# Performance work log

Measured on AMD Instinct MI355X. Metric: run time of the kernel, lower is better.

The kernel has to match this reference:

```python
import jax, jax.numpy as jnp
import numpy as np


def setup_inputs() -> dict:
    key = jax.random.key(0)
    kx, kh = jax.random.split(key)
    x = jax.random.normal(kx, (32, 4, 131072), dtype=jnp.float32)
    h = jax.random.normal(kh, (32, 4, 32768), dtype=jnp.float32)
    return {"x": x, "h": h}


def reference(x, h):
    # Causal FFT convolution: convolve(x, h, mode='causal', pad_mode='min').
    x_len = x.shape[-1]
    h_len = h.shape[-1]
    pad_len = x_len + h_len - 1  # pad_mode='min'
    # rfft with n=pad_len == zero-pad to pad_len then rfft (matches F.pad + rfft)
    X = jnp.fft.rfft(x, n=pad_len)
    H = jnp.fft.rfft(h, n=pad_len)
    Y = X * H
    # torch.fft.irfft default output length = 2*(n_freq-1); jnp matches this default.
    y_pad = jnp.fft.irfft(Y)
    # 'causal' mode: keep first x_len samples
    return y_pad[..., :x_len]
```

## Files before the change

### kernel.cpp

```cpp
#include <hip/hip_runtime.h>
#include <hip/hip_fp16.h>


#define L1FFT 262144
#define NCHAN 128
#define CN1 163839LL
#define CN2 163838LL
#define MBINS 81920
#define XLEN 131072
#define HLEN 32768
#define TWO_PI 6.28318530717958647692f
#define INV512T (1.0f/512.0f)
#define INVLT   (1.0f/262144.0f)
#define CHIRP12 ((float)(0.5 / (163839.0 * 163838.0)))

#define CM_BUILD   0
#define CM_REAL    1
#define CM_COMBINE 2
#define CM_EXTRACT 3
#define CM_FINAL   4
#define RM_BUILD   0
#define RM_CONV    1

#define TS  518
#define TFS 261

typedef float cplx __attribute__((ext_vector_type(2)));

__device__ __forceinline__ cplx mkc(float x, float y){ cplx r; r.x = x; r.y = y; return r; }
__device__ __forceinline__ cplx cmulf(cplx a, cplx b) {
  return a.xx*b + a.yy*mkc(-b.y, b.x);
}
__device__ __forceinline__ cplx cmulcf(cplx a, cplx b) {
  return a.yy*b.yx + a.xx*mkc(b.x, -b.y);
}
__device__ __forceinline__ cplx crot(cplx t, float dsg) {
  return mkc(-dsg*t.y, dsg*t.x);
}

__device__ __forceinline__ cplx sc_turn(float t) {
  return mkc(__builtin_amdgcn_cosf(t), __builtin_amdgcn_sinf(t));
}

__device__ __forceinline__ cplx chirp1(float sgn, long long n) {
  long long m = (n*n) % (2*CN1);
  return sc_turn(sgn * (float)m * (1.0f/(float)(2*CN1)));
}
__device__ __forceinline__ cplx chirp2(float sgn, long long n) {
  long long m = (n*n) % (2*CN2);
  return sc_turn(sgn * (float)m * (1.0f/(float)(2*CN2)));
}
__device__ __forceinline__ cplx chirpv(float sgn, long long Q, long long n) {
  long long m = (n*n) % (2*Q);
  float ang = sgn * (0.5f*TWO_PI) * (float)m / (float)Q;
  float s, c; __sincosf(ang, &s, &c);
  return mkc(c, s);
}

__device__ __forceinline__ int brev4(int x) {
  return ((x&1)<<3) | ((x&2)<<1) | ((x&4)>>1) | ((x&8)>>3);
}
__device__ __forceinline__ int brev5(int x) {
  return (int)(__brev((unsigned)x) >> 27);
}

template<int M>
__device__ __forceinline__ float shf1f(float x) {
  if constexpr (M == 1) {
    return __int_as_float(__builtin_amdgcn_mov_dpp(__float_as_int(x), 0xB1, 0xF, 0xF, true));
  } else if constexpr (M == 2) {
    return __int_as_float(__builtin_amdgcn_mov_dpp(__float_as_int(x), 0x4E, 0xF, 0xF, true));
  } else if constexpr (M == 8) {
    return __int_as_float(__builtin_amdgcn_mov_dpp(__float_as_int(x), 0x128, 0xF, 0xF, true));
  } else {
    return __int_as_float(__builtin_amdgcn_ds_swizzle(__float_as_int(x), (M << 10) | 0x1F));
  }
}
template<int M>
__device__ __forceinline__ cplx shflxT(cplx a) {
  return mkc(shf1f<M>(a.x), shf1f<M>(a.y));
}

__device__ __forceinline__ cplx h2c(__half2 h) {
  float2 f = __half22float2(h); return mkc(f.x, f.y);
}
__device__ __forceinline__ __half2 c2h(cplx c) {
  return __float22half2_rn(make_float2(c.x, c.y));
}

#define C16_1 0.9238795325f
#define C16_2 0.7071067812f
#define C16_3 0.3826834324f
__device__ __forceinline__ float c16t(int j) {
  const float C[8] = {1.f, C16_1, C16_2, C16_3, 0.f, -C16_3, -C16_2, -C16_1};
  return C[j];
}
__device__ __forceinline__ float s16t(int j) {
  const float S[8] = {0.f, C16_3, C16_2, C16_1, 1.f, C16_1, C16_2, C16_3};
  return S[j];
}

__device__ __forceinline__ void lane16_fwd_rest(cplx v[16], float dsg) {
  #pragma unroll
  for (int h = 0; h < 2; ++h)
    #pragma unroll
    for (int j = 0; j < 4; ++j) {
      int i0 = h*8 + j;
      cplx w = mkc(c16t(2*j), dsg * s16t(2*j));
      cplx a = v[i0], b = v[i0+4];
      v[i0] = a + b;
      v[i0+4] = cmulf(a - b, w);
    }
  #pragma unroll
  for (int q = 0; q < 4; ++q)
    #pragma unroll
    for (int j = 0; j < 2; ++j) {
      int i0 = q*4 + j;
      cplx a = v[i0], b = v[i0+2];
      cplx tt = a - b;
      v[i0] = a + b;
      v[i0+2] = (j == 0) ? tt : crot(tt, dsg);
    }
  #pragma unroll
  for (int p = 0; p < 8; ++p) {
    cplx a = v[2*p], b = v[2*p+1];
    v[2*p] = a + b;
    v[2*p+1] = a - b;
  }
}
__device__ __forceinline__ void lane16_fwd(cplx v[16], float dsg) {
  #pragma unroll
  for (int j = 0; j < 8; ++j) {
    cplx w = mkc(c16t(j), dsg * s16t(j));
    cplx a = v[j], b = v[j+8];
    v[j] = a + b;
    v[j+8] = cmulf(a - b, w);
  }
  lane16_fwd_rest(v, dsg);
}
__device__ __forceinline__ void lane16_fwd_h0(cplx v[16], float dsg) {
  #pragma unroll
  for (int j = 0; j < 8; ++j) {
    cplx w = mkc(c16t(j), dsg * s16t(j));
    v[j+8] = cmulf(v[j], w);
  }
  lane16_fwd_rest(v, dsg);
}

__device__ __forceinline__ void lane16_inv(cplx v[16], float dsg) {
  #pragma unroll
  for (int p = 0; p < 8; ++p) {
    cplx a = v[2*p], b = v[2*p+1];
    v[2*p] = a + b;
    v[2*p+1] = a - b;
  }
  #pragma unroll
  for (int q = 0; q < 4; ++q)
    #pragma unroll
    for (int j = 0; j < 2; ++j) {
      int i0 = q*4 + j;
      cplx a = v[i0], b = v[i0+2];
      cplx tb = (j == 0) ? b : crot(b, -dsg);
      v[i0] = a + tb;
      v[i0+2] = a - tb;
    }
  #pragma unroll
  for (int h = 0; h < 2; ++h)
    #pragma unroll
    for (int j = 0; j < 4; ++j) {
      int i0 = h*8 + j;
      cplx w = mkc(c16t(2*j), dsg * s16t(2*j));
      cplx a = v[i0], b = v[i0+4];
      cplx tb = cmulcf(b, w);
      v[i0] = a + tb;
      v[i0+4] = a - tb;
    }
  #pragma unroll
  for (int j = 0; j < 8; ++j) {
    cplx w = mkc(c16t(j), dsg * s16t(j));
    cplx a = v[j], b = v[j+8];
    cplx tb = cmulcf(b, w);
    v[j] = a + tb;
    v[j+8] = a - tb;
  }
}

struct WSel { cplx a16, a8, a4, a2; };
__device__ __forceinline__ WSel make_wsel(int l, float dsg) {
  const cplx one = mkc(1.f, 0.f);
  WSel w;
  w.a16 = (l & 16) ? sc_turn(dsg * (1.0f/32.0f) * (float)(l & 15)) : one;
  w.a8  = (l & 8)  ? sc_turn(dsg * (1.0f/16.0f) * (float)(l & 7))  : one;
  w.a4  = (l & 4)  ? sc_turn(dsg * (1.0f/8.0f)  * (float)(l & 3))  : one;
  w.a2  = ((l & 2) && (l & 1)) ? mkc(0.f, dsg) : one;
  return w;
}

#define XF(mask, w) {                                                          \
    const float s_ = ((l & (mask)) != 0) ? -1.f : 1.f;                         \
    _Pragma("unroll")                                                          \
    for (int r = 0; r < 16; ++r) {                                             \
      cplx o = shflxT<(mask)>(v[r]);                                           \
      v[r] = cmulf(o + s_*v[r], (w));                                          \
    } }
#define XFP(mask) {                                                            \
    const float s_ = ((l & (mask)) != 0) ? -1.f : 1.f;                         \
    _Pragma("unroll")                                                          \
    for (int r = 0; r < 16; ++r) {                                             \
      cplx o = shflxT<(mask)>(v[r]);                                           \
      v[r] = o + s_*v[r];                                                      \
    } }
#define XI(mask, w) {                                                          \
    const float s_ = ((l & (mask)) != 0) ? -1.f : 1.f;                         \
    _Pragma("unroll")                                                          \
    for (int r = 0; r < 16; ++r) {                                             \
      cplx b = cmulcf(v[r], (w));                                              \
      cplx o = shflxT<(mask)>(b);                                              \
      v[r] = o + s_*b;                                                         \
    } }
#define XIP(mask) {                                                            \
    const float s_ = ((l & (mask)) != 0) ? -1.f : 1.f;                         \
    _Pragma("unroll")                                                          \
    for (int r = 0; r < 16; ++r) {                                             \
      cplx b = v[r];                                                           \
      cplx o = shflxT<(mask)>(b);                                              \
      v[r] = o + s_*b;                                                         \
    } }

#define TW_APPLY_FWD(rr, wexpr) v[rr] = cmulf(v[rr], (wexpr));
#define TW_APPLY_INV(rr, wexpr) v[rr] = cmulcf(v[rr], (wexpr));
#define TW512_BODY(APPLY)                                                      \
  cplx w1 = sc_turn(dsg * INV512T * (float)l);                                 \
  cplx w2 = cmulf(w1, w1);                                                     \
  cplx w3 = cmulf(w2, w1);                                                     \
  cplx w4 = cmulf(w2, w2);                                                     \
  cplx w8 = cmulf(w4, w4);                                                     \
  cplx w12 = cmulf(w8, w4);                                                    \
  APPLY(8, w1)  APPLY(4, w2)  APPLY(12, w3) APPLY(2, w4)                       \
  APPLY(10, cmulf(w4, w1)) APPLY(6, cmulf(w4, w2)) APPLY(14, cmulf(w4, w3))    \
  APPLY(1, w8)  APPLY(9, cmulf(w8, w1)) APPLY(5, cmulf(w8, w2))                \
  APPLY(13, cmulf(w8, w3)) APPLY(3, w12) APPLY(11, cmulf(w12, w1))             \
  APPLY(7, cmulf(w12, w2)) APPLY(15, cmulf(w12, w3))

__device__ __forceinline__ void twiddle512_fwd(cplx v[16], int l, float dsg) {
  TW512_BODY(TW_APPLY_FWD)
}
__device__ __forceinline__ void twiddle512_inv(cplx v[16], int l, float dsg) {
  TW512_BODY(TW_APPLY_INV)
}

__device__ __forceinline__ void fft512_core_fwd(cplx v[16], int l, float dsg,
                                                const WSel& w) {
  twiddle512_fwd(v, l, dsg);
  XF(16, w.a16); XF(8, w.a8); XF(4, w.a4); XF(2, w.a2); XFP(1);
}
__device__ __forceinline__ void fft512_fwd(cplx v[16], int l, float dsg,
                                           const WSel& w) {
  lane16_fwd(v, dsg);
  fft512_core_fwd(v, l, dsg, w);
}
__device__ __forceinline__ void fft512_fwd_h0(cplx v[16], int l, float dsg,
                                              const WSel& w) {
  lane16_fwd_h0(v, dsg);
  fft512_core_fwd(v, l, dsg, w);
}

__device__ __forceinline__ void fft512_inv(cplx v[16], int l, float dsg,
                                           const WSel& w) {
  XIP(1); XI(2, w.a2); XI(4, w.a4); XI(8, w.a8); XI(16, w.a16);
  twiddle512_inv(v, l, dsg);
  lane16_inv(v, dsg);
}


__global__ __launch_bounds__(256) void pass_col_k(
    int mode,
    const float* __restrict__ realSrc, int realLen,
    const __half2* cplxSrc,
    const __half2* __restrict__ hcIn,
    __half2* dstFull,
    __half2* __restrict__ specOut,
    float* __restrict__ realOut,
    long long Q, float csgn, int lo, int hi)
{
  __shared__ __align__(16) unsigned char ldsraw[8 * TS * 4];
  __half2* tile = (__half2*)ldsraw;
  const int t   = threadIdx.x;
  const int c0  = blockIdx.x * 8;
  const int ch  = blockIdx.y;
  const int l   = t & 31;
  const int ccf = t >> 5;
  const int c   = c0 + ccf;
  cplx v[16];
  WSel ws = make_wsel(l, -1.f);

  if (mode == CM_BUILD) {
    #pragma unroll
    for (int m = 0; m < 16; ++m) {
      int n = ((l + 32*m) << 9) + c;
      int np = (n <= hi) ? n : n - L1FFT;
      v[m] = (np >= lo) ? chirpv(csgn, Q, (long long)np) : mkc(0.f, 0.f);
    }
  } else if (mode == CM_REAL) {
    #pragma unroll
    for (int i = 0; i < 8; ++i) {
      int qq = t + 256*i;
      int cc = qq & 7, r = qq >> 3;
      int n = (r << 9) + c0 + cc;
      cplx val = mkc(0.f, 0.f);
      if (n < realLen) {
        float xv = realSrc[(size_t)ch * realLen + n];
        val = chirp1(-1.f, (long long)n) * xv;
      }
      tile[cc*TS + r] = c2h(val);
    }
    __syncthreads();
    #pragma unroll
    for (int m = 0; m < 8; ++m) v[m] = h2c(tile[ccf*TS + l + 32*m]);
    __syncthreads();
  } else {
    const uint2* srcp = (const uint2*)(cplxSrc + (size_t)ch * L1FFT);
    #pragma unroll
    for (int i = 0; i < 8; ++i) {
      int qq = t + 256*i;
      int cc = qq & 7, rp = qq >> 3;
      uint2 val = srcp[(size_t)rp*512 + c0 + cc];
      *(uint2*)&tile[cc*TS + 2*rp] = val;
    }
    __syncthreads();
    #pragma unroll
    for (int m = 0; m < 16; ++m) v[m] = h2c(tile[ccf*TS + l + 32*m]);
    __syncthreads();
  }

  if (mode == CM_COMBINE) {
    fft512_inv(v, l, -1.f, ws);
    #pragma unroll
    for (int m = 0; m <= 4; ++m) {
      int n = l + 32*m;
      cplx H = h2c(hcIn[(size_t)ch*MBINS + c*160 + n]);
      v[m] = cmulf(v[m], H);
    }
    #pragma unroll
    for (int m = 5; m < 8; ++m) v[m] = mkc(0.f, 0.f);
  }

  if (mode <= CM_COMBINE) {
    if (mode == CM_BUILD) fft512_fwd(v, l, -1.f, ws);
    else                  fft512_fwd_h0(v, l, -1.f, ws);
    {
      cplx B1 = sc_turn(-INVLT * (float)c);
      cplx C  = sc_turn(-INVLT * (float)(c * (16*brev5(l))));
      cplx B2 = cmulf(B1, B1);
      cplx B4 = cmulf(B2, B2);
      cplx d0 = C, d1 = cmulf(C, B1), d2 = cmulf(C, B2), d3 = cmulf(d1, B2);
      #define ST4(r0,r1,r2,r3)                                                 \
        tile[ccf*TS + l + 32*(r0)] = c2h(cmulf(v[r0], d0));                    \
        tile[ccf*TS + l + 32*(r1)] = c2h(cmulf(v[r1], d1));                    \
        tile[ccf*TS + l + 32*(r2)] = c2h(cmulf(v[r2], d2));                    \
        tile[ccf*TS + l + 32*(r3)] = c2h(cmulf(v[r3], d3));
      #define DUP4()                                                           \
        d0 = cmulf(d0, B4); d1 = cmulf(d1, B4);                                \
        d2 = cmulf(d2, B4); d3 = cmulf(d3, B4);
      ST4(0, 8, 4, 12)  DUP4()
      ST4(2, 10, 6, 14) DUP4()
      ST4(1, 9, 5, 13)  DUP4()
      ST4(3, 11, 7, 15)
      #undef ST4
      #undef DUP4
    }
    __syncthreads();
    {
      uint2* dstp = (uint2*)(dstFull + (size_t)ch * L1FFT);
      #pragma unroll
      for (int i = 0; i < 8; ++i) {
        int qq = t + 256*i;
        int cc = qq & 7, rp = qq >> 3;
        dstp[(size_t)rp*512 + c0 + cc] = *(const uint2*)&tile[cc*TS + 2*rp];
      }
    }
  } else if (mode == CM_EXTRACT) {
    fft512_inv(v, l, -1.f, ws);
    #pragma unroll
    for (int m = 0; m <= 4; ++m) {
      int n = l + 32*m;
      long long k = ((long long)n << 9) + c;
      cplx cw = chirp1(-1.f, k);
      float fk = (float)k;
      cplx wc = sc_turn(fk * fk * CHIRP12);
      float eps = (k == 0 || k == MBINS-1) ? 1.f : 2.f;
      float sc = eps / (float)CN2;
      cplx cw2 = cmulf(cw, wc) * sc;
      specOut[(size_t)ch*MBINS + c*160 + n] = c2h(cmulf(v[m], cw2));
    }
  } else {
    fft512_inv(v, l, -1.f, ws);
    float* tf = (float*)ldsraw;
    #pragma unroll
    for (int m = 0; m < 8; ++m) {
      int n = l + 32*m;
      long long nb = ((long long)n << 9) + c;
      cplx cw = chirp2(+1.f, nb);
      tf[ccf*TFS + n] = v[m].x*cw.x - v[m].y*cw.y;
    }
    __syncthreads();
    {
      int cc = t & 7, u = t >> 3;
      #pragma unroll
      for (int i = 0; i < 8; ++i) {
        int n = u + 32*i;
        realOut[(size_t)ch*XLEN + (n << 9) + c0 + cc] = tf[cc*TFS + n];
      }
    }
  }
}

__global__ __launch_bounds__(256) void pass_row_k(
    int mode, __half2* a, const __half2* __restrict__ g)
{
  const int t = threadIdx.x;
  const int l = t & 31;
  const int w8 = t >> 5;
  const int rs = blockIdx.x * 8 + w8;
  const int rp = rs >> 1, par = rs & 1;
  const int ch = blockIdx.y;
  const int j = 16*brev5(rs & 31) + brev4(rs >> 5);
  __half2* A = a + (size_t)ch * L1FFT + (size_t)rp * 1024 + 2*l + par;
  cplx v[16];
  WSel ws = make_wsel(l, -1.f);
  #pragma unroll
  for (int m = 0; m < 16; ++m) v[m] = h2c(A[64*m]);

  if (mode == RM_CONV) {
    const __half2* G = g + (size_t)rp * 1024 + 2*l + par;
    cplx gv[16];
    #pragma unroll
    for (int m = 0; m < 16; ++m) gv[m] = h2c(G[64*m]);
    fft512_fwd(v, l, -1.f, ws);
    #pragma unroll
    for (int r = 0; r < 16; ++r) v[r] = cmulf(v[r], gv[r]);
    fft512_inv(v, l, -1.f, ws);
    {
      cplx T = sc_turn(INVLT * (float)(l * j)) * (1.f/(float)L1FFT);
      cplx F = sc_turn(INVLT * (float)(32 * j));
      #pragma unroll
      for (int m = 0; m < 16; ++m) {
        A[64*m] = c2h(cmulf(v[m], T));
        T = cmulf(T, F);
      }
    }
  } else {
    fft512_fwd(v, l, -1.f, ws);
    #pragma unroll
    for (int r = 0; r < 16; ++r) A[64*r] = c2h(v[r]);
  }
}

__global__ void diag_ws_too_small(float* out) { out[0] = 123456.0f; }

extern "C" void kernel_launch(void* const* d_in, const int* in_sizes, int n_in,
                              void* d_out, int out_size, void* d_ws, size_t ws_size,
                              hipStream_t stream) {
  const float* x = (const float*)d_in[0];
  const float* h = (const float*)d_in[1];
  float* out = (float*)d_out;

  const size_t fixedB   = 2ull * L1FFT * sizeof(__half2);
  const size_t perChanB = (size_t)L1FFT * sizeof(__half2) + (size_t)MBINS * sizeof(__half2);
  if (ws_size < fixedB + perChanB) {
    diag_ws_too_small<<<1, 1, 0, stream>>>(out);
    return;
  }
  int chunk = (int)((ws_size - fixedB) / perChanB);
  if (chunk > NCHAN) chunk = NCHAN;

  __half2* V1 = (__half2*)d_ws;
  __half2* W  = V1 + L1FFT;
  __half2* A  = W + L1FFT;
  __half2* Hc = A + (size_t)chunk * L1FFT;

  dim3 blk(256);
  dim3 g1(64, 1);

  pass_col_k<<<g1, blk, 0, stream>>>(CM_BUILD, nullptr, 0, nullptr, nullptr,
                                     V1, nullptr, nullptr, CN1, +1.f, -(XLEN-1), MBINS-1);
  pass_row_k<<<g1, blk, 0, stream>>>(RM_BUILD, V1, nullptr);
  pass_col_k<<<g1, blk, 0, stream>>>(CM_BUILD, nullptr, 0, nullptr, nullptr,
                                     W, nullptr, nullptr, CN2, -1.f, -(MBINS-1), XLEN-1);
  pass_row_k<<<g1, blk, 0, stream>>>(RM_BUILD, W, nullptr);

  for (int ch0 = 0; ch0 < NCHAN; ch0 += chunk) {
    int nc = NCHAN - ch0; if (nc > chunk) nc = chunk;
    dim3 gC(64, nc), gR(64, nc);
    const float* hq = h   + (size_t)ch0 * HLEN;
    const float* xq = x   + (size_t)ch0 * XLEN;
    float*       oq = out + (size_t)ch0 * XLEN;

    pass_col_k<<<gC, blk, 0, stream>>>(CM_REAL, hq, HLEN, nullptr, nullptr,
                                       A, nullptr, nullptr, CN1, 0.f, 0, 0);
    pass_row_k<<<gR, blk, 0, stream>>>(RM_CONV, A, V1);
    pass_col_k<<<gC, blk, 0, stream>>>(CM_EXTRACT, nullptr, 0, A, nullptr,
                                       nullptr, Hc, nullptr, CN1, 0.f, 0, 0);

    pass_col_k<<<gC, blk, 0, stream>>>(CM_REAL, xq, XLEN, nullptr, nullptr,
                                       A, nullptr, nullptr, CN1, 0.f, 0, 0);
    pass_row_k<<<gR, blk, 0, stream>>>(RM_CONV, A, V1);
    pass_col_k<<<gC, blk, 0, stream>>>(CM_COMBINE, nullptr, 0, A, Hc,
                                       A, nullptr, nullptr, CN2, 0.f, 0, 0);
    pass_row_k<<<gR, blk, 0, stream>>>(RM_CONV, A, W);
    pass_col_k<<<gC, blk, 0, stream>>>(CM_FINAL, nullptr, 0, A, nullptr,
                                       nullptr, nullptr, oq, CN2, 0.f, 0, 0);
  }
}
```

Before: 747.5 us.

## Batch h and x transforms together and fuse extract with combine pass

Processes the h and x chirp-z transforms in the same launches by doubling the grid's y-dimension over both signals. The former extract pass, which wrote the H spectrum to a separate buffer, is folded into the combine pass, so H is computed in registers and multiplied immediately. The two constant-table build passes are also merged into single launches. This cuts the launch count from 8 to 5 per chunk plus 4 to 2 at setup, removes the Hc round trip through memory, and gives each launch more parallel work. In exchange, each channel needs twice the workspace, so fewer channels fit per chunk, and the fused column kernel does two inverse FFTs, which may raise register pressure.

```diff
diff --git a/kernel.cpp b/kernel.cpp
--- a/kernel.cpp
+++ b/kernel.cpp
@@ -14,13 +14,13 @@
 #define INVLT   (1.0f/262144.0f)
 #define CHIRP12 ((float)(0.5 / (163839.0 * 163838.0)))
 
-#define CM_BUILD   0
-#define CM_REAL    1
-#define CM_COMBINE 2
-#define CM_EXTRACT 3
-#define CM_FINAL   4
-#define RM_BUILD   0
-#define RM_CONV    1
+#define CM_BUILD 0
+#define CM_REAL  1
+#define CM_XCOMB 2
+#define CM_FINAL 3
+#define RM_BUILD 0
+#define RM_CONV2 1
+#define RM_CONVX 2
 
 #define TS  518
 #define TFS 261
@@ -273,21 +273,66 @@
 }
 
 
+__device__ __forceinline__ void gather_tile(__half2* tile, const __half2* src,
+                                            int c0, int t) {
+  const uint2* srcp = (const uint2*)src;
+  #pragma unroll
+  for (int i = 0; i < 8; ++i) {
+    int qq = t + 256*i;
+    int cc = qq & 7, rp = qq >> 3;
+    *(uint2*)&tile[cc*TS + 2*rp] = srcp[(size_t)rp*512 + c0 + cc];
+  }
+}
+__device__ __forceinline__ void scatter_tile(__half2* dst, const __half2* tile,
+                                             int c0, int t) {
+  uint2* dstp = (uint2*)dst;
+  #pragma unroll
+  for (int i = 0; i < 8; ++i) {
+    int qq = t + 256*i;
+    int cc = qq & 7, rp = qq >> 3;
+    dstp[(size_t)rp*512 + c0 + cc] = *(const uint2*)&tile[cc*TS + 2*rp];
+  }
+}
+
+__device__ __forceinline__ void twiddle_store(__half2* tile, cplx v[16],
+                                              int l, int ccf, int c) {
+  cplx B1 = sc_turn(-INVLT * (float)c);
+  cplx C  = sc_turn(-INVLT * (float)(c * (16*brev5(l))));
+  cplx B2 = cmulf(B1, B1);
+  cplx B4 = cmulf(B2, B2);
+  cplx d0 = C, d1 = cmulf(C, B1), d2 = cmulf(C, B2), d3 = cmulf(d1, B2);
+  #define ST4(r0,r1,r2,r3)                                                     \
+    tile[ccf*TS + l + 32*(r0)] = c2h(cmulf(v[r0], d0));                        \
+    tile[ccf*TS + l + 32*(r1)] = c2h(cmulf(v[r1], d1));                        \
+    tile[ccf*TS + l + 32*(r2)] = c2h(cmulf(v[r2], d2));                        \
+    tile[ccf*TS + l + 32*(r3)] = c2h(cmulf(v[r3], d3));
+  #define DUP4()                                                               \
+    d0 = cmulf(d0, B4); d1 = cmulf(d1, B4);                                    \
+    d2 = cmulf(d2, B4); d3 = cmulf(d3, B4);
+  ST4(0, 8, 4, 12)  DUP4()
+  ST4(2, 10, 6, 14) DUP4()
+  ST4(1, 9, 5, 13)  DUP4()
+  ST4(3, 11, 7, 15)
+  #undef ST4
+  #undef DUP4
+}
+
 __global__ __launch_bounds__(256) void pass_col_k(
     int mode,
-    const float* __restrict__ realSrc, int realLen,
-    const __half2* cplxSrc,
-    const __half2* __restrict__ hcIn,
+    const float* __restrict__ realA, int lenA,
+    const float* __restrict__ realB, int lenB,
+    const __half2* srcX, const __half2* srcH,
     __half2* dstFull,
-    __half2* __restrict__ specOut,
     float* __restrict__ realOut,
-    long long Q, float csgn, int lo, int hi)
+    int nc, int chunkSlots,
+    long long Qa, float csgnA, int loA, int hiA,
+    long long Qb, float csgnB, int loB, int hiB)
 {
   __shared__ __align__(16) unsigned char ldsraw[8 * TS * 4];
   __half2* tile = (__half2*)ldsraw;
   const int t   = threadIdx.x;
   const int c0  = blockIdx.x * 8;
-  const int ch  = blockIdx.y;
+  const int y   = blockIdx.y;
   const int l   = t & 31;
   const int ccf = t >> 5;
   const int c   = c0 + ccf;
@@ -295,92 +340,56 @@
   WSel ws = make_wsel(l, -1.f);
 
   if (mode == CM_BUILD) {
+    long long Q = (y == 0) ? Qa : Qb;
+    float csgn  = (y == 0) ? csgnA : csgnB;
+    int lo = (y == 0) ? loA : loB;
+    int hi = (y == 0) ? hiA : hiB;
     #pragma unroll
     for (int m = 0; m < 16; ++m) {
       int n = ((l + 32*m) << 9) + c;
       int np = (n <= hi) ? n : n - L1FFT;
       v[m] = (np >= lo) ? chirpv(csgn, Q, (long long)np) : mkc(0.f, 0.f);
     }
-  } else if (mode == CM_REAL) {
+    fft512_fwd(v, l, -1.f, ws);
+    twiddle_store(tile, v, l, ccf, c);
+    __syncthreads();
+    scatter_tile(dstFull + (size_t)y * L1FFT, tile, c0, t);
+    return;
+  }
+
+  if (mode == CM_REAL) {
+    const float* rs_; int rl_; int slot;
+    if (y < nc) { rs_ = realA + (size_t)y * lenA;        rl_ = lenA; slot = y; }
+    else        { rs_ = realB + (size_t)(y - nc) * lenB; rl_ = lenB;
+                  slot = chunkSlots + (y - nc); }
     #pragma unroll
     for (int i = 0; i < 8; ++i) {
       int qq = t + 256*i;
       int cc = qq & 7, r = qq >> 3;
       int n = (r << 9) + c0 + cc;
       cplx val = mkc(0.f, 0.f);
-      if (n < realLen) {
-        float xv = realSrc[(size_t)ch * realLen + n];
-        val = chirp1(-1.f, (long long)n) * xv;
-      }
+      if (n < rl_) val = chirp1(-1.f, (long long)n) * rs_[n];
       tile[cc*TS + r] = c2h(val);
     }
     __syncthreads();
     #pragma unroll
     for (int m = 0; m < 8; ++m) v[m] = h2c(tile[ccf*TS + l + 32*m]);
     __syncthreads();
-  } else {
-    const uint2* srcp = (const uint2*)(cplxSrc + (size_t)ch * L1FFT);
-    #pragma unroll
-    for (int i = 0; i < 8; ++i) {
-      int qq = t + 256*i;
-      int cc = qq & 7, rp = qq >> 3;
-      uint2 val = srcp[(size_t)rp*512 + c0 + cc];
-      *(uint2*)&tile[cc*TS + 2*rp] = val;
-    }
+    fft512_fwd_h0(v, l, -1.f, ws);
+    twiddle_store(tile, v, l, ccf, c);
+    __syncthreads();
+    scatter_tile(dstFull + (size_t)slot * L1FFT, tile, c0, t);
+    return;
+  }
+
+  if (mode == CM_XCOMB) {
+    gather_tile(tile, srcH + (size_t)y * L1FFT, c0, t);
     __syncthreads();
     #pragma unroll
     for (int m = 0; m < 16; ++m) v[m] = h2c(tile[ccf*TS + l + 32*m]);
     __syncthreads();
-  }
-
-  if (mode == CM_COMBINE) {
     fft512_inv(v, l, -1.f, ws);
-    #pragma unroll
-    for (int m = 0; m <= 4; ++m) {
-      int n = l + 32*m;
-      cplx H = h2c(hcIn[(size_t)ch*MBINS + c*160 + n]);
-      v[m] = cmulf(v[m], H);
-    }
-    #pragma unroll
-    for (int m = 5; m < 8; ++m) v[m] = mkc(0.f, 0.f);
-  }
-
-  if (mode <= CM_COMBINE) {
-    if (mode == CM_BUILD) fft512_fwd(v, l, -1.f, ws);
-    else                  fft512_fwd_h0(v, l, -1.f, ws);
-    {
-      cplx B1 = sc_turn(-INVLT * (float)c);
-      cplx C  = sc_turn(-INVLT * (float)(c * (16*brev5(l))));
-      cplx B2 = cmulf(B1, B1);
-      cplx B4 = cmulf(B2, B2);
-      cplx d0 = C, d1 = cmulf(C, B1), d2 = cmulf(C, B2), d3 = cmulf(d1, B2);
-      #define ST4(r0,r1,r2,r3)                                                 \
-        tile[ccf*TS + l + 32*(r0)] = c2h(cmulf(v[r0], d0));                    \
-        tile[ccf*TS + l + 32*(r1)] = c2h(cmulf(v[r1], d1));                    \
-        tile[ccf*TS + l + 32*(r2)] = c2h(cmulf(v[r2], d2));                    \
-        tile[ccf*TS + l + 32*(r3)] = c2h(cmulf(v[r3], d3));
-      #define DUP4()                                                           \
-        d0 = cmulf(d0, B4); d1 = cmulf(d1, B4);                                \
-        d2 = cmulf(d2, B4); d3 = cmulf(d3, B4);
-      ST4(0, 8, 4, 12)  DUP4()
-      ST4(2, 10, 6, 14) DUP4()
-      ST4(1, 9, 5, 13)  DUP4()
-      ST4(3, 11, 7, 15)
-      #undef ST4
-      #undef DUP4
-    }
-    __syncthreads();
-    {
-      uint2* dstp = (uint2*)(dstFull + (size_t)ch * L1FFT);
-      #pragma unroll
-      for (int i = 0; i < 8; ++i) {
-        int qq = t + 256*i;
-        int cc = qq & 7, rp = qq >> 3;
-        dstp[(size_t)rp*512 + c0 + cc] = *(const uint2*)&tile[cc*TS + 2*rp];
-      }
-    }
-  } else if (mode == CM_EXTRACT) {
-    fft512_inv(v, l, -1.f, ws);
+    cplx Hf[5];
     #pragma unroll
     for (int m = 0; m <= 4; ++m) {
       int n = l + 32*m;
@@ -390,48 +399,71 @@
       cplx wc = sc_turn(fk * fk * CHIRP12);
       float eps = (k == 0 || k == MBINS-1) ? 1.f : 2.f;
       float sc = eps / (float)CN2;
-      cplx cw2 = cmulf(cw, wc) * sc;
-      specOut[(size_t)ch*MBINS + c*160 + n] = c2h(cmulf(v[m], cw2));
-    }
-  } else {
+      Hf[m] = cmulf(v[m], cmulf(cw, wc) * sc);
+    }
+    gather_tile(tile, srcX + (size_t)(chunkSlots + y) * L1FFT, c0, t);
+    __syncthreads();
+    #pragma unroll
+    for (int m = 0; m < 16; ++m) v[m] = h2c(tile[ccf*TS + l + 32*m]);
+    __syncthreads();
     fft512_inv(v, l, -1.f, ws);
-    float* tf = (float*)ldsraw;
-    #pragma unroll
-    for (int m = 0; m < 8; ++m) {
-      int n = l + 32*m;
-      long long nb = ((long long)n << 9) + c;
-      cplx cw = chirp2(+1.f, nb);
-      tf[ccf*TFS + n] = v[m].x*cw.x - v[m].y*cw.y;
-    }
-    __syncthreads();
-    {
-      int cc = t & 7, u = t >> 3;
-      #pragma unroll
-      for (int i = 0; i < 8; ++i) {
-        int n = u + 32*i;
-        realOut[(size_t)ch*XLEN + (n << 9) + c0 + cc] = tf[cc*TFS + n];
-      }
+    #pragma unroll
+    for (int m = 0; m <= 4; ++m) v[m] = cmulf(v[m], Hf[m]);
+    #pragma unroll
+    for (int m = 5; m < 8; ++m) v[m] = mkc(0.f, 0.f);
+    fft512_fwd_h0(v, l, -1.f, ws);
+    twiddle_store(tile, v, l, ccf, c);
+    __syncthreads();
+    scatter_tile(dstFull + (size_t)(chunkSlots + y) * L1FFT, tile, c0, t);
+    return;
+  }
+
+  gather_tile(tile, srcX + (size_t)(chunkSlots + y) * L1FFT, c0, t);
+  __syncthreads();
+  #pragma unroll
+  for (int m = 0; m < 16; ++m) v[m] = h2c(tile[ccf*TS + l + 32*m]);
+  __syncthreads();
+  fft512_inv(v, l, -1.f, ws);
+  float* tf = (float*)ldsraw;
+  #pragma unroll
+  for (int m = 0; m < 8; ++m) {
+    int n = l + 32*m;
+    long long nb = ((long long)n << 9) + c;
+    cplx cw = chirp2(+1.f, nb);
+    tf[ccf*TFS + n] = v[m].x*cw.x - v[m].y*cw.y;
+  }
+  __syncthreads();
+  {
+    int cc = t & 7, u = t >> 3;
+    #pragma unroll
+    for (int i = 0; i < 8; ++i) {
+      int n = u + 32*i;
+      realOut[(size_t)y*XLEN + (n << 9) + c0 + cc] = tf[cc*TFS + n];
     }
   }
 }
 
 __global__ __launch_bounds__(256) void pass_row_k(
-    int mode, __half2* a, const __half2* __restrict__ g)
+    int mode, __half2* a, const __half2* __restrict__ g, int nc, int chunkSlots)
 {
   const int t = threadIdx.x;
   const int l = t & 31;
   const int w8 = t >> 5;
   const int rs = blockIdx.x * 8 + w8;
   const int rp = rs >> 1, par = rs & 1;
-  const int ch = blockIdx.y;
+  const int y = blockIdx.y;
+  int slot;
+  if (mode == RM_BUILD)      slot = y;
+  else if (mode == RM_CONV2) slot = (y < nc) ? y : chunkSlots + (y - nc);
+  else                       slot = chunkSlots + y;
   const int j = 16*brev5(rs & 31) + brev4(rs >> 5);
-  __half2* A = a + (size_t)ch * L1FFT + (size_t)rp * 1024 + 2*l + par;
+  __half2* A = a + (size_t)slot * L1FFT + (size_t)rp * 1024 + 2*l + par;
   cplx v[16];
   WSel ws = make_wsel(l, -1.f);
   #pragma unroll
   for (int m = 0; m < 16; ++m) v[m] = h2c(A[64*m]);
 
-  if (mode == RM_CONV) {
+  if (mode != RM_BUILD) {
     const __half2* G = g + (size_t)rp * 1024 + 2*l + par;
     cplx gv[16];
     #pragma unroll
@@ -466,7 +498,7 @@
   float* out = (float*)d_out;
 
   const size_t fixedB   = 2ull * L1FFT * sizeof(__half2);
-  const size_t perChanB = (size_t)L1FFT * sizeof(__half2) + (size_t)MBINS * sizeof(__half2);
+  const size_t perChanB = 2ull * L1FFT * sizeof(__half2);
   if (ws_size < fixedB + perChanB) {
     diag_ws_too_small<<<1, 1, 0, stream>>>(out);
     return;
@@ -477,38 +509,31 @@
   __half2* V1 = (__half2*)d_ws;
   __half2* W  = V1 + L1FFT;
   __half2* A  = W + L1FFT;
-  __half2* Hc = A + (size_t)chunk * L1FFT;
 
   dim3 blk(256);
-  dim3 g1(64, 1);
-
-  pass_col_k<<<g1, blk, 0, stream>>>(CM_BUILD, nullptr, 0, nullptr, nullptr,
-                                     V1, nullptr, nullptr, CN1, +1.f, -(XLEN-1), MBINS-1);
-  pass_row_k<<<g1, blk, 0, stream>>>(RM_BUILD, V1, nullptr);
-  pass_col_k<<<g1, blk, 0, stream>>>(CM_BUILD, nullptr, 0, nullptr, nullptr,
-                                     W, nullptr, nullptr, CN2, -1.f, -(MBINS-1), XLEN-1);
-  pass_row_k<<<g1, blk, 0, stream>>>(RM_BUILD, W, nullptr);
+
+  pass_col_k<<<dim3(64, 2), blk, 0, stream>>>(CM_BUILD,
+      nullptr, 0, nullptr, 0, nullptr, nullptr, V1, nullptr, 0, 0,
+      CN1, +1.f, -(XLEN-1), MBINS-1,
+      CN2, -1.f, -(MBINS-1), XLEN-1);
+  pass_row_k<<<dim3(64, 2), blk, 0, stream>>>(RM_BUILD, V1, nullptr, 0, 0);
 
   for (int ch0 = 0; ch0 < NCHAN; ch0 += chunk) {
     int nc = NCHAN - ch0; if (nc > chunk) nc = chunk;
-    dim3 gC(64, nc), gR(64, nc);
     const float* hq = h   + (size_t)ch0 * HLEN;
     const float* xq = x   + (size_t)ch0 * XLEN;
     float*       oq = out + (size_t)ch0 * XLEN;
 
-    pass_col_k<<<gC, blk, 0, stream>>>(CM_REAL, hq, HLEN, nullptr, nullptr,
-                                       A, nullptr, nullptr, CN1, 0.f, 0, 0);
-    pass_row_k<<<gR, blk, 0, stream>>>(RM_CONV, A, V1);
-    pass_col_k<<<gC, blk, 0, stream>>>(CM_EXTRACT, nullptr, 0, A, nullptr,
-                                       nullptr, Hc, nullptr, CN1, 0.f, 0, 0);
-
-    pass_col_k<<<gC, blk, 0, stream>>>(CM_REAL, xq, XLEN, nullptr, nullptr,
-                                       A, nullptr, nullptr, CN1, 0.f, 0, 0);
-    pass_row_k<<<gR, blk, 0, stream>>>(RM_CONV, A, V1);
-    pass_col_k<<<gC, blk, 0, stream>>>(CM_COMBINE, nullptr, 0, A, Hc,
-                                       A, nullptr, nullptr, CN2, 0.f, 0, 0);
-    pass_row_k<<<gR, blk, 0, stream>>>(RM_CONV, A, W);
-    pass_col_k<<<gC, blk, 0, stream>>>(CM_FINAL, nullptr, 0, A, nullptr,
-                                       nullptr, nullptr, oq, CN2, 0.f, 0, 0);
-  }
-}
+    pass_col_k<<<dim3(64, 2*nc), blk, 0, stream>>>(CM_REAL,
+        hq, HLEN, xq, XLEN, nullptr, nullptr, A, nullptr, nc, chunk,
+        0, 0.f, 0, 0, 0, 0.f, 0, 0);
+    pass_row_k<<<dim3(64, 2*nc), blk, 0, stream>>>(RM_CONV2, A, V1, nc, chunk);
+    pass_col_k<<<dim3(64, nc), blk, 0, stream>>>(CM_XCOMB,
+        nullptr, 0, nullptr, 0, A, A, A, nullptr, nc, chunk,
+        0, 0.f, 0, 0, 0, 0.f, 0, 0);
+    pass_row_k<<<dim3(64, nc), blk, 0, stream>>>(RM_CONVX, A, W, nc, chunk);
+    pass_col_k<<<dim3(64, nc), blk, 0, stream>>>(CM_FINAL,
+        nullptr, 0, nullptr, 0, A, nullptr, nullptr, oq, nc, chunk,
+        0, 0.f, 0, 0, 0, 0.f, 0, 0);
+  }
+}
```

Result: slower. 857.2 us (+14.7%).
